# Performance work log

Measured on AMD Instinct MI355X. Metric: run time of the kernel, lower is better.

Reference implementation:

```python
import jax, jax.numpy as jnp
import numpy as np

D_MODEL = 1024
HEAD_DIM = 128
SEQ_LEN = 4096
BATCH = 4


def setup_inputs() -> dict:
    key = jax.random.key(0)
    kx, kq, kk, kv, ko = jax.random.split(key, 5)
    s = 1.0 / np.sqrt(D_MODEL)
    so = 1.0 / np.sqrt(HEAD_DIM)
    return {
        "x": jax.random.normal(kx, (SEQ_LEN, BATCH, D_MODEL), dtype=jnp.float32),
        "Wq": jax.random.uniform(kq, (HEAD_DIM, D_MODEL), jnp.float32, -s, s),
        "Wk": jax.random.uniform(kk, (HEAD_DIM, D_MODEL), jnp.float32, -s, s),
        "Wv": jax.random.uniform(kv, (HEAD_DIM, D_MODEL), jnp.float32, -s, s),
        "Wo": jax.random.uniform(ko, (D_MODEL, HEAD_DIM), jnp.float32, -so, so),
    }


def reference(x, Wq, Wk, Wv, Wo):
    # x: (S, B, D)
    S = x.shape[0]
    scale = Wq.shape[0] ** (-0.5)  # head_dim ** -0.5
    # Projections (Linear: x @ W.T) -> (B, S, H)
    Q = jnp.einsum('sbd,hd->bsh', x, Wq)
    K = jnp.einsum('sbd,hd->bsh', x, Wk)
    V = jnp.einsum('sbd,hd->bsh', x, Wv)
    scores = jnp.einsum('bqh,bkh->bqk', Q, K) * scale  # (B, S, S)
    causal = jnp.tril(jnp.ones((S, S), dtype=bool))
    scores = jnp.where(causal[None], scores, -jnp.inf)
    attn = jax.nn.softmax(scores, axis=-1)
    attn = jnp.nan_to_num(attn, nan=0.0)
    out = jnp.einsum('bqk,bkh->bqh', attn, V)  # (B, S, H)
    # out_proj then back to (S, B, D)
    return jnp.einsum('bsh,dh->sbd', out, Wo)
```

## Files before the change

kernel.cpp:

```cpp
#include <hip/hip_runtime.h>
#include <hip/hip_bf16.h>

#define S_LEN 4096
#define BATCH 4
#define DMODEL 1024
#define HDIM 128
#define NSLOT 8

typedef __attribute__((ext_vector_type(8))) short short8;
typedef __attribute__((ext_vector_type(4))) short short4v;
typedef __attribute__((ext_vector_type(4))) float float4v;
typedef __attribute__((ext_vector_type(16))) float float16v;
typedef __attribute__((ext_vector_type(4))) int int4v;

#define MASKVAL (-3.0e38f)
#define MINIT   (-1.0e30f)

static __device__ __forceinline__ unsigned short f2bf(float f) {
    __hip_bfloat16 h = __float2bfloat16(f);
    return *reinterpret_cast<unsigned short*>(&h);
}
static __device__ __forceinline__ unsigned short f2h(float f) {
    _Float16 h = (_Float16)f; return *reinterpret_cast<unsigned short*>(&h);
}
static __device__ __forceinline__ float h2f(unsigned short u) {
    _Float16 h = *reinterpret_cast<_Float16*>(&u); return (float)h;
}
static __device__ __forceinline__ short8 ldf(const unsigned short* p) {
    return *reinterpret_cast<const short8*>(p);
}
static __device__ __forceinline__ short8 pack_p(const float* pv, int hi) {
    unsigned int A  = (unsigned int)f2bf(pv[0]) | ((unsigned int)f2bf(pv[1]) << 16);
    unsigned int Bw = (unsigned int)f2bf(pv[2]) | ((unsigned int)f2bf(pv[3]) << 16);
    unsigned int C  = (unsigned int)f2bf(pv[4]) | ((unsigned int)f2bf(pv[5]) << 16);
    unsigned int D  = (unsigned int)f2bf(pv[6]) | ((unsigned int)f2bf(pv[7]) << 16);
    unsigned int y1 = (unsigned int)__shfl_xor((int)(hi ? A : C), 32);
    unsigned int y2 = (unsigned int)__shfl_xor((int)(hi ? Bw : D), 32);
    int4v pw;
    pw[0] = (int)(hi ? y1 : A);
    pw[1] = (int)(hi ? y2 : Bw);
    pw[2] = (int)(hi ? C : y1);
    pw[3] = (int)(hi ? D : y2);
    union { int4v iv; short8 s; } pu; pu.iv = pw;
    return pu.s;
}

__global__ __launch_bounds__(256) void xprep_kernel(
    const float* __restrict__ x, unsigned short* __restrict__ xf)
{
    int n = blockIdx.x * 256 + threadIdx.x;
    int b = n >> 17;
    int rem = n & 131071;
    int sb = rem >> 10;
    int rem2 = rem & 1023;
    int kq = rem2 >> 4;
    int grp = rem2 & 15;
    int lane0 = grp * 4;
    int par = grp >> 3;
    int s0 = lane0 & 31;
    int k = kq * 16 + par * 8;

    short8 hv[4];
#pragma unroll
    for (int r = 0; r < 4; r++) {
        int s = sb * 32 + s0 + r;
        const float* src = &x[((size_t)s * BATCH + b) * DMODEL + k];
        float4 v0 = *reinterpret_cast<const float4*>(src);
        float4 v1 = *reinterpret_cast<const float4*>(src + 4);
        short8 h;
        h[0] = (short)f2bf(v0.x); h[1] = (short)f2bf(v0.y);
        h[2] = (short)f2bf(v0.z); h[3] = (short)f2bf(v0.w);
        h[4] = (short)f2bf(v1.x); h[5] = (short)f2bf(v1.y);
        h[6] = (short)f2bf(v1.z); h[7] = (short)f2bf(v1.w);
        hv[r] = h;
    }
    size_t addr = (((size_t)b * 128 + sb) * 64 + kq) * 512 + (size_t)lane0 * 8;
#pragma unroll
    for (int r = 0; r < 4; r++)
        *reinterpret_cast<short8*>(xf + addr + r * 8) = hv[r];
}

__global__ __launch_bounds__(256) void wprep_kernel(
    const float* __restrict__ Wq, const float* __restrict__ Wk,
    const float* __restrict__ Wv, unsigned short* __restrict__ Wqf,
    unsigned short* __restrict__ Wkf, unsigned short* __restrict__ Wvf)
{
    const int which = blockIdx.y;
    const float* W = (which == 0) ? Wq : (which == 1) ? Wk : Wv;
    unsigned short* Wf = (which == 0) ? Wqf : (which == 1) ? Wkf : Wvf;
    int n = blockIdx.x * 256 + threadIdx.x;
    int d = n >> 7, k8 = n & 127;
    const float* src = &W[(size_t)d * DMODEL + k8 * 8];
    float4 v0 = *reinterpret_cast<const float4*>(src);
    float4 v1 = *reinterpret_cast<const float4*>(src + 4);
    short8 h;
    h[0] = (short)f2bf(v0.x); h[1] = (short)f2bf(v0.y);
    h[2] = (short)f2bf(v0.z); h[3] = (short)f2bf(v0.w);
    h[4] = (short)f2bf(v1.x); h[5] = (short)f2bf(v1.y);
    h[6] = (short)f2bf(v1.z); h[7] = (short)f2bf(v1.w);
    size_t addr = (((size_t)(d >> 5)) * 64 + (k8 >> 1)) * 512
                + (size_t)(((d & 31) + 32 * (k8 & 1)) * 8);
    *reinterpret_cast<short8*>(Wf + addr) = h;
}

__global__ __launch_bounds__(256) void qkv_gemm_kernel(
    const unsigned short* __restrict__ xf, const unsigned short* __restrict__ Wqf,
    const unsigned short* __restrict__ Wkf, const unsigned short* __restrict__ Wvf,
    unsigned short* __restrict__ Qf, unsigned short* __restrict__ Kf,
    unsigned short* __restrict__ Vf)
{
    __shared__ float cacc[2 * 4096];

    const int t = threadIdx.x;
    const int w = t >> 6;
    const int lane = t & 63;
    const int hi = lane >> 5;
    const int tloc = w & 1;
    const int half = w >> 1;
    const int tile = blockIdx.x * 2 + tloc;
    const int which = tile >> 9;
    const int rem = tile & 511;
    const int b = rem >> 7;
    const int sblk = rem & 127;

    const unsigned short* Wf = (which == 0) ? Wqf : (which == 1) ? Wkf : Wvf;
    const unsigned short* xp =
        xf + (((size_t)b * 128 + sblk) * 64 + half * 32) * 512 + lane * 8;
    const unsigned short* wp = Wf + (size_t)half * 32 * 512 + lane * 8;

    float16v acc[4];
#pragma unroll
    for (int i = 0; i < 4; i++)
#pragma unroll
        for (int r = 0; r < 16; r++) acc[i][r] = 0.f;

    {
        short8 xA = ldf(xp);
        short8 wA[4];
#pragma unroll
        for (int d4 = 0; d4 < 4; d4++) wA[d4] = ldf(wp + (size_t)(d4 * 64) * 512);
        for (int ks = 0; ks < 32; ks++) {
            short8 xB = xA;
            short8 wB[4];
#pragma unroll
            for (int d4 = 0; d4 < 4; d4++) wB[d4] = wA[d4];
            if (ks < 31) {
                xB = ldf(xp + (ks + 1) * 512);
#pragma unroll
                for (int d4 = 0; d4 < 4; d4++)
                    wB[d4] = ldf(wp + (size_t)(d4 * 64 + ks + 1) * 512);
            }
            __builtin_amdgcn_s_setprio(1);
            if (which != 2) {
#pragma unroll
                for (int d4 = 0; d4 < 4; d4++)
                    acc[d4] = __builtin_amdgcn_mfma_f32_32x32x16_bf16(
                        wA[d4], xA, acc[d4], 0, 0, 0);
            } else {
#pragma unroll
                for (int d4 = 0; d4 < 4; d4++)
                    acc[d4] = __builtin_amdgcn_mfma_f32_32x32x16_bf16(
                        xA, wA[d4], acc[d4], 0, 0, 0);
            }
            __builtin_amdgcn_s_setprio(0);
            xA = xB;
#pragma unroll
            for (int d4 = 0; d4 < 4; d4++) wA[d4] = wB[d4];
        }
    }

    float* my = cacc + tloc * 4096;
    if (half == 1) {
#pragma unroll
        for (int db = 0; db < 4; db++)
#pragma unroll
            for (int rc = 0; rc < 4; rc++) {
                float4v v;
#pragma unroll
                for (int j = 0; j < 4; j++) v[j] = acc[db][rc * 4 + j];
                *reinterpret_cast<float4v*>(
                    my + (db * 4 + rc) * 256 + lane * 4) = v;
            }
    }
    __syncthreads();
    if (half != 0) return;

#pragma unroll
    for (int db = 0; db < 4; db++)
#pragma unroll
        for (int rc = 0; rc < 4; rc++) {
            float4v v = *reinterpret_cast<const float4v*>(
                my + (db * 4 + rc) * 256 + lane * 4);
#pragma unroll
            for (int j = 0; j < 4; j++) acc[db][rc * 4 + j] += v[j];
        }

    if (which != 2) {
        unsigned short* Of = (which == 0) ? Qf : Kf;
        const float scale = (which == 0) ? 0.08838834764831845f : 1.0f;
#pragma unroll
        for (int db = 0; db < 4; db++)
#pragma unroll
            for (int g = 0; g < 4; g++) {
                int f = db * 2 + (g >> 1);
                size_t addr = (((size_t)b * 128 + sblk) * 8 + f) * 512
                            + (size_t)(((lane & 31) + 32 * (g & 1)) * 8 + 4 * hi);
                short4v ov;
#pragma unroll
                for (int j = 0; j < 4; j++)
                    ov[j] = (short)f2bf(acc[db][g * 4 + j] * scale);
                *reinterpret_cast<short4v*>(Of + addr) = ov;
            }
    } else {
#pragma unroll
        for (int hb = 0; hb < 4; hb++)
#pragma unroll
            for (int g = 0; g < 4; g++) {
                int kt16 = sblk * 2 + (g >> 1);
                size_t addr = (((size_t)b * 256 + kt16) * 4 + hb) * 512
                            + (size_t)(((lane & 31) + 32 * (g & 1)) * 8 + 4 * hi);
                short4v ov;
#pragma unroll
                for (int j = 0; j < 4; j++)
                    ov[j] = (short)f2bf(acc[hb][g * 4 + j]);
                *reinterpret_cast<short4v*>(Vf + addr) = ov;
            }
    }
}

__global__ __launch_bounds__(256) void attn_kernel(
    const unsigned short* __restrict__ Qf, const unsigned short* __restrict__ Kf,
    const unsigned short* __restrict__ Vf, unsigned short* __restrict__ Opart,
    float* __restrict__ Mpart, float* __restrict__ Lpart)
{
    const int t = threadIdx.x;
    const int w = t >> 6;
    const int lane = t & 63;
    const int l31 = lane & 31;
    const int hi = lane >> 5;

    const int i = blockIdx.x;
    const int xx = i & 7;
    const int b = xx >> 1;
    const int p = (i >> 3) * 2 + (xx & 1);
    const int qt = 31 - (p & 31);
    const int c = p >> 5;

    const int nkv = 2 * (qt + 1);
    const int lo = c * 8;
    if (lo >= nkv) return;
    const int hic = min(lo + 8, nkv);

    const int qb = qt * 128;
    const int qrow = qb + w * 32 + l31;
    const int lastblk = (qb + w * 32 + 31) >> 6;
    const int myhi = min(hic, lastblk + 1);

    const unsigned short* qp =
        Qf + (((size_t)b * 128 + (qt * 4 + w)) * 8) * 512 + lane * 8;
    short8 qf[8];
#pragma unroll
    for (int f = 0; f < 8; f++) qf[f] = ldf(qp + f * 512);

    const unsigned short* kbase =
        Kf + (size_t)b * (S_LEN / 32) * 8 * 512 + lane * 8;
    const unsigned short* vbase =
        Vf + (size_t)b * (S_LEN / 16) * 4 * 512 + lane * 8;

    float m_run = MINIT, l_run = 0.f;
    float16v o[4];
#pragma unroll
    for (int hb = 0; hb < 4; hb++)
#pragma unroll
        for (int r = 0; r < 16; r++) o[hb][r] = 0.f;

    for (int ti = lo; ti < myhi; ti++) {
        const int kvb = ti * 64;
        const unsigned short* kp = kbase + (size_t)ti * 8192;
        const unsigned short* vp = vbase + (size_t)ti * 8192;

        short8 ka[4], kb[4], va[4], vb[4];
#pragma unroll
        for (int j = 0; j < 4; j++) ka[j] = ldf(kp + j * 512);
#pragma unroll
        for (int j = 0; j < 4; j++) kb[j] = ldf(kp + (4 + j) * 512);

        float16v s0, s1;
#pragma unroll
        for (int r = 0; r < 16; r++) { s0[r] = 0.f; s1[r] = 0.f; }

        __builtin_amdgcn_s_setprio(1);
#pragma unroll
        for (int j = 0; j < 4; j++)
            s0 = __builtin_amdgcn_mfma_f32_32x32x16_bf16(ka[j], qf[j], s0, 0, 0, 0);
        __builtin_amdgcn_s_setprio(0);
#pragma unroll
        for (int j = 0; j < 4; j++) ka[j] = ldf(kp + 4096 + j * 512);
        __builtin_amdgcn_s_setprio(1);
#pragma unroll
        for (int j = 0; j < 4; j++)
            s0 = __builtin_amdgcn_mfma_f32_32x32x16_bf16(kb[j], qf[4 + j], s0, 0, 0, 0);
        __builtin_amdgcn_s_setprio(0);
#pragma unroll
        for (int j = 0; j < 4; j++) kb[j] = ldf(kp + 4096 + (4 + j) * 512);
        __builtin_amdgcn_s_setprio(1);
#pragma unroll
        for (int j = 0; j < 4; j++)
            s1 = __builtin_amdgcn_mfma_f32_32x32x16_bf16(ka[j], qf[j], s1, 0, 0, 0);
        __builtin_amdgcn_s_setprio(0);
#pragma unroll
        for (int j = 0; j < 4; j++) va[j] = ldf(vp + j * 512);
        __builtin_amdgcn_s_setprio(1);
#pragma unroll
        for (int j = 0; j < 4; j++)
            s1 = __builtin_amdgcn_mfma_f32_32x32x16_bf16(kb[j], qf[4 + j], s1, 0, 0, 0);
        __builtin_amdgcn_s_setprio(0);
#pragma unroll
        for (int j = 0; j < 4; j++) vb[j] = ldf(vp + (4 + j) * 512);

        if (kvb + 63 > qb + w * 32) {
#pragma unroll
            for (int r = 0; r < 16; r++) {
                int kv0 = kvb + (r & 3) + 8 * (r >> 2) + 4 * hi;
                if (kv0 > qrow) s0[r] = MASKVAL;
                if (kv0 + 32 > qrow) s1[r] = MASKVAL;
            }
        }

        float mx[16];
#pragma unroll
        for (int r = 0; r < 16; r++) mx[r] = fmaxf(s0[r], s1[r]);
#pragma unroll
        for (int st = 8; st >= 1; st >>= 1)
#pragma unroll
            for (int r = 0; r < st; r++) mx[r] = fmaxf(mx[r], mx[r + st]);
        float pmax = fmaxf(mx[0], __shfl_xor(mx[0], 32));
        if (!__all(pmax - m_run <= 8.0f)) {
            float mnew = fmaxf(m_run, pmax);
            float alpha = __expf(m_run - mnew);
            l_run *= alpha;
#pragma unroll
            for (int hb = 0; hb < 4; hb++) o[hb] = o[hb] * alpha;
            m_run = mnew;
        }
#pragma unroll
        for (int r = 0; r < 16; r++) s0[r] = __expf(s0[r] - m_run);
#pragma unroll
        for (int r = 0; r < 16; r++) s1[r] = __expf(s1[r] - m_run);
        float sm[16];
#pragma unroll
        for (int r = 0; r < 16; r++) sm[r] = s0[r] + s1[r];
#pragma unroll
        for (int st = 8; st >= 1; st >>= 1)
#pragma unroll
            for (int r = 0; r < st; r++) sm[r] += sm[r + st];
        l_run += sm[0] + __shfl_xor(sm[0], 32);

        float t0[8], t1[8], t2[8], t3[8];
#pragma unroll
        for (int j = 0; j < 8; j++) { t0[j] = s0[j]; t1[j] = s0[8 + j]; }
#pragma unroll
        for (int j = 0; j < 8; j++) { t2[j] = s1[j]; t3[j] = s1[8 + j]; }

#pragma unroll
        for (int j = 0; j < 4; j++) ka[j] = ldf(vp + (8 + j) * 512);
        short8 p0 = pack_p(t0, hi);
        __builtin_amdgcn_s_setprio(1);
#pragma unroll
        for (int hb = 0; hb < 4; hb++)
            o[hb] = __builtin_amdgcn_mfma_f32_32x32x16_bf16(va[hb], p0, o[hb], 0, 0, 0);
        __builtin_amdgcn_s_setprio(0);
#pragma unroll
        for (int j = 0; j < 4; j++) kb[j] = ldf(vp + (12 + j) * 512);
        short8 p1 = pack_p(t1, hi);
        __builtin_amdgcn_s_setprio(1);
#pragma unroll
        for (int hb = 0; hb < 4; hb++)
            o[hb] = __builtin_amdgcn_mfma_f32_32x32x16_bf16(vb[hb], p1, o[hb], 0, 0, 0);
        short8 p2 = pack_p(t2, hi);
#pragma unroll
        for (int hb = 0; hb < 4; hb++)
            o[hb] = __builtin_amdgcn_mfma_f32_32x32x16_bf16(ka[hb], p2, o[hb], 0, 0, 0);
        short8 p3 = pack_p(t3, hi);
#pragma unroll
        for (int hb = 0; hb < 4; hb++)
            o[hb] = __builtin_amdgcn_mfma_f32_32x32x16_bf16(kb[hb], p3, o[hb], 0, 0, 0);
        __builtin_amdgcn_s_setprio(0);
    }

    const size_t R0 = (size_t)(c * BATCH + b) * S_LEN;
    const float inv = (l_run > 0.f) ? 1.f / l_run : 0.f;
#pragma unroll
    for (int hb = 0; hb < 4; hb++)
#pragma unroll
        for (int g = 0; g < 4; g++) {
            int h0 = hb * 32 + g * 8 + hi * 4;
            short4v ov;
#pragma unroll
            for (int jj = 0; jj < 4; jj++)
                ov[jj] = (short)f2h(o[hb][g * 4 + jj] * inv);
            *reinterpret_cast<short4v*>(&Opart[(R0 + qrow) * HDIM + h0]) = ov;
        }
    if (hi == 0) { Mpart[R0 + qrow] = m_run; Lpart[R0 + qrow] = l_run; }
}

__global__ __launch_bounds__(256) void combine_kernel(
    const unsigned short* __restrict__ Opart, const float* __restrict__ Mpart,
    const float* __restrict__ Lpart, unsigned short* __restrict__ Ob)
{
    const int BS = BATCH * S_LEN;
    int idx = blockIdx.x * 256 + threadIdx.x;
    int r = idx >> 4, hc = (idx & 15) * 8;
    int q = r & (S_LEN - 1);
    int qt = q >> 7;
    int nkv = 2 * (qt + 1);
    int cnt = (nkv + 7) >> 3;

    float m = -INFINITY;
    for (int j = 0; j < cnt; j++) m = fmaxf(m, Mpart[j * BS + r]);
    float wsum = 0.f;
    float acc[8];
#pragma unroll
    for (int e = 0; e < 8; e++) acc[e] = 0.f;
    for (int j = 0; j < cnt; j++) {
        float wj = __expf(Mpart[j * BS + r] - m) * Lpart[j * BS + r];
        wsum += wj;
        short8 o = *reinterpret_cast<const short8*>(
            &Opart[((size_t)j * BS + r) * HDIM + hc]);
#pragma unroll
        for (int e = 0; e < 8; e++) acc[e] += wj * h2f((unsigned short)o[e]);
    }
    float inv = 1.f / wsum;
    short8 ob;
#pragma unroll
    for (int e = 0; e < 8; e++) ob[e] = (short)f2bf(acc[e] * inv);
    *reinterpret_cast<short8*>(&Ob[(size_t)r * HDIM + hc]) = ob;
}

__global__ __launch_bounds__(256) void out_proj_kernel(
    const unsigned short* __restrict__ Ob, const float* __restrict__ Wo,
    float* __restrict__ out)
{
    __shared__ unsigned short As[128 * 128];
    __shared__ unsigned short Bs[128 * 128];

    const int t = threadIdx.x;
    const int lane = t & 63, w = t >> 6;
    const int l15 = lane & 15, l4 = lane >> 4;
    const int wr = (w >> 1) * 64, wc = (w & 1) * 64;
    const int s0 = blockIdx.x * 128;
    const int d0 = blockIdx.y * 128;
    const int b = blockIdx.z;

#pragma unroll
    for (int p = 0; p < 8; p++) {
        int e = p * 2048 + t * 8;
        int r = e >> 7, h = e & 127;
        short8 v = *reinterpret_cast<const short8*>(
            &Ob[((size_t)b * S_LEN + s0 + r) * HDIM + h]);
        int off = (r * 256 + h * 2) ^ ((r & 7) << 4);
        *reinterpret_cast<short8*>(reinterpret_cast<char*>(As) + off) = v;
    }
#pragma unroll
    for (int p = 0; p < 16; p++) {
        int e = p * 1024 + t * 4;
        int r = e >> 7, h = e & 127;
        float4 v = *reinterpret_cast<const float4*>(&Wo[(size_t)(d0 + r) * HDIM + h]);
        short4v hh;
        hh[0] = (short)f2bf(v.x); hh[1] = (short)f2bf(v.y);
        hh[2] = (short)f2bf(v.z); hh[3] = (short)f2bf(v.w);
        int off = (r * 256 + h * 2) ^ ((r & 7) << 4);
        *reinterpret_cast<short4v*>(reinterpret_cast<char*>(Bs) + off) = hh;
    }
    __syncthreads();

    float4v acc[4][4];
#pragma unroll
    for (int i = 0; i < 4; i++)
#pragma unroll
        for (int j = 0; j < 4; j++) acc[i][j] = (float4v){0.f, 0.f, 0.f, 0.f};

#pragma unroll
    for (int kk = 0; kk < 4; kk++) {
        short8 a[4], bf[4];
#pragma unroll
        for (int mi = 0; mi < 4; mi++) {
            int row = wr + mi * 16 + l15;
            int off = (row * 256 + (kk * 32 + l4 * 8) * 2) ^ ((row & 7) << 4);
            a[mi] = *reinterpret_cast<const short8*>(
                reinterpret_cast<const char*>(As) + off);
        }
#pragma unroll
        for (int ni = 0; ni < 4; ni++) {
            int row = wc + ni * 16 + l15;
            int off = (row * 256 + (kk * 32 + l4 * 8) * 2) ^ ((row & 7) << 4);
            bf[ni] = *reinterpret_cast<const short8*>(
                reinterpret_cast<const char*>(Bs) + off);
        }
#pragma unroll
        for (int mi = 0; mi < 4; mi++)
#pragma unroll
            for (int ni = 0; ni < 4; ni++)
                acc[mi][ni] = __builtin_amdgcn_mfma_f32_16x16x32_bf16(
                    a[mi], bf[ni], acc[mi][ni], 0, 0, 0);
    }

#pragma unroll
    for (int mi = 0; mi < 4; mi++)
#pragma unroll
        for (int ni = 0; ni < 4; ni++)
#pragma unroll
            for (int r = 0; r < 4; r++) {
                int s = s0 + wr + mi * 16 + l4 * 4 + r;
                int d = d0 + wc + ni * 16 + l15;
                out[((size_t)s * BATCH + b) * DMODEL + d] = acc[mi][ni][r];
            }
}

extern "C" void kernel_launch(void* const* d_in, const int* in_sizes, int n_in,
                              void* d_out, int out_size, void* d_ws, size_t ws_size,
                              hipStream_t stream) {
    const float* x  = (const float*)d_in[0];
    const float* Wq = (const float*)d_in[1];
    const float* Wk = (const float*)d_in[2];
    const float* Wv = (const float*)d_in[3];
    const float* Wo = (const float*)d_in[4];
    float* out = (float*)d_out;

    const size_t BS = (size_t)BATCH * S_LEN;
    unsigned short* xf    = (unsigned short*)d_ws;
    unsigned short* Opart = (unsigned short*)d_ws;
    float* Mpart = (float*)((char*)d_ws + (32u << 20));
    float* Lpart = Mpart + NSLOT * BS;
    unsigned short* Wqf = (unsigned short*)((char*)d_ws + (33u << 20));
    unsigned short* Wkf = Wqf + 131072;
    unsigned short* Wvf = Wkf + 131072;
    unsigned short* Qf  = Wvf + 131072;
    unsigned short* Kf  = Qf + 2097152;
    unsigned short* Vf  = Kf + 2097152;
    unsigned short* Ob  = Vf + 2097152;

    xprep_kernel<<<2048, 256, 0, stream>>>(x, xf);
    wprep_kernel<<<dim3(64, 3), 256, 0, stream>>>(Wq, Wk, Wv, Wqf, Wkf, Wvf);
    qkv_gemm_kernel<<<768, 256, 0, stream>>>(xf, Wqf, Wkf, Wvf, Qf, Kf, Vf);
    attn_kernel<<<1024, 256, 0, stream>>>(Qf, Kf, Vf, Opart, Mpart, Lpart);
    combine_kernel<<<1024, 256, 0, stream>>>(Opart, Mpart, Lpart, Ob);
    out_proj_kernel<<<dim3(32, 8, BATCH), 256, 0, stream>>>(Ob, Wo, out);
}
```

Before: 126.7 us.

## Compact attention grid to valid chunks and prefetch next K tile across iterations

The block-to-(query tile, chunk) mapping now enumerates only valid chunks through a small loop, so the launch shrinks from 1024 to 576 blocks with no early-exit blocks. The first K fragment of the next KV tile is loaded during the PV MFMAs of the current iteration, hiding its latency across loop iterations. The cost is extra register pressure from the kn buffer and a redundant load on the last iteration.

```diff
diff --git a/kernel.cpp b/kernel.cpp
--- a/kernel.cpp
+++ b/kernel.cpp
@@ -242,13 +242,17 @@
     const int i = blockIdx.x;
     const int xx = i & 7;
     const int b = xx >> 1;
-    const int p = (i >> 3) * 2 + (xx & 1);
-    const int qt = 31 - (p & 31);
-    const int c = p >> 5;
+    int j = (i >> 3) * 2 + (xx & 1);
+    int qt = 31;
+    while (true) {
+        int cnt = (qt + 4) >> 2;
+        if (j < cnt) break;
+        j -= cnt; qt--;
+    }
+    const int c = j;
 
     const int nkv = 2 * (qt + 1);
     const int lo = c * 8;
-    if (lo >= nkv) return;
     const int hic = min(lo + 8, nkv);
 
     const int qb = qt * 128;
@@ -274,16 +278,23 @@
 #pragma unroll
         for (int r = 0; r < 16; r++) o[hb][r] = 0.f;
 
+    short8 kn[4];
+    {
+        const unsigned short* kp0 = kbase + (size_t)lo * 8192;
+#pragma unroll
+        for (int jj = 0; jj < 4; jj++) kn[jj] = ldf(kp0 + jj * 512);
+    }
+
     for (int ti = lo; ti < myhi; ti++) {
         const int kvb = ti * 64;
         const unsigned short* kp = kbase + (size_t)ti * 8192;
         const unsigned short* vp = vbase + (size_t)ti * 8192;
+        const unsigned short* kpn =
+            kbase + (size_t)((ti + 1 < myhi) ? ti + 1 : ti) * 8192;
 
         short8 ka[4], kb[4], va[4], vb[4];
 #pragma unroll
-        for (int j = 0; j < 4; j++) ka[j] = ldf(kp + j * 512);
-#pragma unroll
-        for (int j = 0; j < 4; j++) kb[j] = ldf(kp + (4 + j) * 512);
+        for (int jj = 0; jj < 4; jj++) kb[jj] = ldf(kp + (4 + jj) * 512);
 
         float16v s0, s1;
 #pragma unroll
@@ -291,32 +302,32 @@
 
         __builtin_amdgcn_s_setprio(1);
 #pragma unroll
-        for (int j = 0; j < 4; j++)
-            s0 = __builtin_amdgcn_mfma_f32_32x32x16_bf16(ka[j], qf[j], s0, 0, 0, 0);
-        __builtin_amdgcn_s_setprio(0);
-#pragma unroll
-        for (int j = 0; j < 4; j++) ka[j] = ldf(kp + 4096 + j * 512);
-        __builtin_amdgcn_s_setprio(1);
-#pragma unroll
-        for (int j = 0; j < 4; j++)
-            s0 = __builtin_amdgcn_mfma_f32_32x32x16_bf16(kb[j], qf[4 + j], s0, 0, 0, 0);
-        __builtin_amdgcn_s_setprio(0);
-#pragma unroll
-        for (int j = 0; j < 4; j++) kb[j] = ldf(kp + 4096 + (4 + j) * 512);
-        __builtin_amdgcn_s_setprio(1);
-#pragma unroll
-        for (int j = 0; j < 4; j++)
-            s1 = __builtin_amdgcn_mfma_f32_32x32x16_bf16(ka[j], qf[j], s1, 0, 0, 0);
-        __builtin_amdgcn_s_setprio(0);
-#pragma unroll
-        for (int j = 0; j < 4; j++) va[j] = ldf(vp + j * 512);
-        __builtin_amdgcn_s_setprio(1);
-#pragma unroll
-        for (int j = 0; j < 4; j++)
-            s1 = __builtin_amdgcn_mfma_f32_32x32x16_bf16(kb[j], qf[4 + j], s1, 0, 0, 0);
-        __builtin_amdgcn_s_setprio(0);
-#pragma unroll
-        for (int j = 0; j < 4; j++) vb[j] = ldf(vp + (4 + j) * 512);
+        for (int jj = 0; jj < 4; jj++)
+            s0 = __builtin_amdgcn_mfma_f32_32x32x16_bf16(kn[jj], qf[jj], s0, 0, 0, 0);
+        __builtin_amdgcn_s_setprio(0);
+#pragma unroll
+        for (int jj = 0; jj < 4; jj++) ka[jj] = ldf(kp + 4096 + jj * 512);
+        __builtin_amdgcn_s_setprio(1);
+#pragma unroll
+        for (int jj = 0; jj < 4; jj++)
+            s0 = __builtin_amdgcn_mfma_f32_32x32x16_bf16(kb[jj], qf[4 + jj], s0, 0, 0, 0);
+        __builtin_amdgcn_s_setprio(0);
+#pragma unroll
+        for (int jj = 0; jj < 4; jj++) kb[jj] = ldf(kp + 4096 + (4 + jj) * 512);
+        __builtin_amdgcn_s_setprio(1);
+#pragma unroll
+        for (int jj = 0; jj < 4; jj++)
+            s1 = __builtin_amdgcn_mfma_f32_32x32x16_bf16(ka[jj], qf[jj], s1, 0, 0, 0);
+        __builtin_amdgcn_s_setprio(0);
+#pragma unroll
+        for (int jj = 0; jj < 4; jj++) va[jj] = ldf(vp + jj * 512);
+        __builtin_amdgcn_s_setprio(1);
+#pragma unroll
+        for (int jj = 0; jj < 4; jj++)
+            s1 = __builtin_amdgcn_mfma_f32_32x32x16_bf16(kb[jj], qf[4 + jj], s1, 0, 0, 0);
+        __builtin_amdgcn_s_setprio(0);
+#pragma unroll
+        for (int jj = 0; jj < 4; jj++) vb[jj] = ldf(vp + (4 + jj) * 512);
 
         if (kvb + 63 > qb + w * 32) {
 #pragma unroll
@@ -358,12 +369,12 @@
 
         float t0[8], t1[8], t2[8], t3[8];
 #pragma unroll
-        for (int j = 0; j < 8; j++) { t0[j] = s0[j]; t1[j] = s0[8 + j]; }
-#pragma unroll
-        for (int j = 0; j < 8; j++) { t2[j] = s1[j]; t3[j] = s1[8 + j]; }
-
-#pragma unroll
-        for (int j = 0; j < 4; j++) ka[j] = ldf(vp + (8 + j) * 512);
+        for (int jj = 0; jj < 8; jj++) { t0[jj] = s0[jj]; t1[jj] = s0[8 + jj]; }
+#pragma unroll
+        for (int jj = 0; jj < 8; jj++) { t2[jj] = s1[jj]; t3[jj] = s1[8 + jj]; }
+
+#pragma unroll
+        for (int jj = 0; jj < 4; jj++) ka[jj] = ldf(vp + (8 + jj) * 512);
         short8 p0 = pack_p(t0, hi);
         __builtin_amdgcn_s_setprio(1);
 #pragma unroll
@@ -371,13 +382,17 @@
             o[hb] = __builtin_amdgcn_mfma_f32_32x32x16_bf16(va[hb], p0, o[hb], 0, 0, 0);
         __builtin_amdgcn_s_setprio(0);
 #pragma unroll
-        for (int j = 0; j < 4; j++) kb[j] = ldf(vp + (12 + j) * 512);
+        for (int jj = 0; jj < 4; jj++) kb[jj] = ldf(vp + (12 + jj) * 512);
         short8 p1 = pack_p(t1, hi);
         __builtin_amdgcn_s_setprio(1);
 #pragma unroll
         for (int hb = 0; hb < 4; hb++)
             o[hb] = __builtin_amdgcn_mfma_f32_32x32x16_bf16(vb[hb], p1, o[hb], 0, 0, 0);
+        __builtin_amdgcn_s_setprio(0);
+#pragma unroll
+        for (int jj = 0; jj < 4; jj++) kn[jj] = ldf(kpn + jj * 512);
         short8 p2 = pack_p(t2, hi);
+        __builtin_amdgcn_s_setprio(1);
 #pragma unroll
         for (int hb = 0; hb < 4; hb++)
             o[hb] = __builtin_amdgcn_mfma_f32_32x32x16_bf16(ka[hb], p2, o[hb], 0, 0, 0);
@@ -543,7 +558,7 @@
     xprep_kernel<<<2048, 256, 0, stream>>>(x, xf);
     wprep_kernel<<<dim3(64, 3), 256, 0, stream>>>(Wq, Wk, Wv, Wqf, Wkf, Wvf);
     qkv_gemm_kernel<<<768, 256, 0, stream>>>(xf, Wqf, Wkf, Wvf, Qf, Kf, Vf);
-    attn_kernel<<<1024, 256, 0, stream>>>(Qf, Kf, Vf, Opart, Mpart, Lpart);
+    attn_kernel<<<576, 256, 0, stream>>>(Qf, Kf, Vf, Opart, Mpart, Lpart);
     combine_kernel<<<1024, 256, 0, stream>>>(Opart, Mpart, Lpart, Ob);
     out_proj_kernel<<<dim3(32, 8, BATCH), 256, 0, stream>>>(Ob, Wo, out);
 }
```

Result: faster. 123.7 us (-2.4%).
